# Performance work log

Measured on AMD Instinct MI355X. Metric: run time of the kernel, lower is better.

Reference implementation:

```python
import jax, jax.numpy as jnp
import numpy as np

MIN_V, MAX_V, NORM = 0.0, 4.0, 4.0
NUM_HEADS = 8
BN_EPS = 1e-5

@jax.custom_vjp
def quant(x):
    return jnp.round(jnp.clip(x, MIN_V, MAX_V))

def _quant_fwd(x):
    return jnp.round(jnp.clip(x, MIN_V, MAX_V)), x

def _quant_bwd(x, g):
    # straight-through: zero grad outside [min, max]
    return (jnp.where((x < MIN_V) | (x > MAX_V), 0.0, g),)

quant.defvjp(_quant_fwd, _quant_bwd)

def spike(x):
    return quant(x) / NORM

def conv_bn(x, w, gamma, beta, mean, var):
    # 1x1 conv (no bias) + BatchNorm2d (eval mode, running stats)
    y = jnp.einsum('oc,bchw->bohw', w, x)
    s = gamma / jnp.sqrt(var + BN_EPS)
    return y * s[None, :, None, None] + (beta - mean * s)[None, :, None, None]


def setup_inputs() -> dict:
    key = jax.random.key(0)
    B, C, H, W = 8, 384, 64, 64
    ks = jax.random.split(key, 21)
    d = {'x': jax.random.normal(ks[0], (B, C, H, W), jnp.float32)}
    i = 1
    for p in ('q', 'k', 'v', 'p'):
        d[f'{p}_w'] = jax.random.normal(ks[i], (C, C), jnp.float32) * 0.05; i += 1
        d[f'{p}_gamma'] = jax.random.uniform(ks[i], (C,), jnp.float32, 0.5, 1.5); i += 1
        d[f'{p}_beta'] = jax.random.normal(ks[i], (C,), jnp.float32) * 0.1; i += 1
        d[f'{p}_mean'] = jax.random.normal(ks[i], (C,), jnp.float32) * 0.1; i += 1
        d[f'{p}_var'] = jax.random.uniform(ks[i], (C,), jnp.float32, 0.5, 1.5); i += 1
    return d


def reference(x, q_w, q_gamma, q_beta, q_mean, q_var,
              k_w, k_gamma, k_beta, k_mean, k_var,
              v_w, v_gamma, v_beta, v_mean, v_var,
              p_w, p_gamma, p_beta, p_mean, p_var):
    B, C, H, W = x.shape
    N = H * W
    hd = C // NUM_HEADS
    scale = hd ** -0.5

    xs = spike(x)
    q = spike(conv_bn(xs, q_w, q_gamma, q_beta, q_mean, q_var))
    k = spike(conv_bn(xs, k_w, k_gamma, k_beta, k_mean, k_var))
    v = spike(conv_bn(xs, v_w, v_gamma, v_beta, v_mean, v_var))

    # (B,C,H,W) -> (B,heads,N,hd); channel c = h*hd + d
    def to_heads(t):
        return t.reshape(B, NUM_HEADS, hd, N).transpose(0, 1, 3, 2)

    q, k, v = to_heads(q), to_heads(k), to_heads(v)

    # softmax-free attention: (q @ k^T) @ v == q @ (k^T @ v)  -> O(N*d^2)
    kv = jnp.einsum('bhnd,bhne->bhde', k, v)          # [B,H,hd,hd]
    attn = jnp.einsum('bhnd,bhde->bhne', q, kv) * (scale * 2)  # [B,H,N,hd]

    # back to (B, C_v, N): torch does transpose(2,3).reshape(B,C_v,N)
    a = attn.transpose(0, 1, 3, 2).reshape(B, C, N)
    a = spike(a).reshape(B, C, H, W)
    out = conv_bn(a, p_w, p_gamma, p_beta, p_mean, p_var)
    return out
```

## Files before the change

kernel.cpp:

```cpp
#include <hip/hip_runtime.h>
#include <stdint.h>

#define B_  8
#define C_  384
#define N_  4096
#define NH_ 8
#define HD_ 48
#define CB_ (C_*N_)
#define KS2 768

typedef __attribute__((ext_vector_type(8))) short short8;
typedef __attribute__((ext_vector_type(8))) _Float16 half8;
typedef __attribute__((ext_vector_type(4))) float f32x4;

struct P5 { const float *w, *g, *be, *mu, *va; };
struct W4 { const float *w0, *w1, *w2, *w3; };

__device__ __forceinline__ float b2f(unsigned short u) {
    union { unsigned int i; float f; } c; c.i = ((unsigned int)u) << 16; return c.f;
}
__device__ __forceinline__ unsigned short f2b(float f) {
    union { float f; unsigned int i; } c; c.f = f;
    return (unsigned short)((c.i + 0x7FFFu + ((c.i >> 16) & 1u)) >> 16);
}
__device__ __forceinline__ unsigned short f2h(float f) {
    union { _Float16 h; unsigned short u; } c; c.h = (_Float16)f; return c.u;
}
__device__ __forceinline__ float spikef(float f) {
    f = fminf(fmaxf(f, 0.0f), 4.0f);
    return rintf(f) * 0.25f;
}
__device__ __forceinline__ void async16(const void* g, void* l) {
    __builtin_amdgcn_global_load_lds((const __attribute__((address_space(1))) void*)g,
                                     (__attribute__((address_space(3))) void*)l, 16, 0, 0);
}

__global__ __launch_bounds__(256) void k_prep(W4 ws4, unsigned short* __restrict__ wsp) {
    int idx = blockIdx.x * 256 + threadIdx.x;
    if (idx >= 589824) return;
    int mat = idx / 147456, rem = idx % 147456;
    int o = rem / 384, c = rem % 384;
    const float* W = (mat == 0) ? ws4.w0 : (mat == 1) ? ws4.w1 : (mat == 2) ? ws4.w2 : ws4.w3;
    float w = W[o * 384 + c];
    _Float16 hh = (fabsf(w) < 6.103515625e-05f) ? (_Float16)0 : (_Float16)w;
    float r1 = w - (float)hh;
    float s  = r1 * 4096.0f;
    union { _Float16 h; unsigned short u; } ch, cl;
    ch.h = hh; cl.h = (_Float16)s;
    unsigned short* row = wsp + (size_t)mat * 384 * KS2 + (size_t)o * KS2 + c;
    row[0] = cl.u; row[384] = ch.u;
}

__global__ __launch_bounds__(256) void k0_spike_T(const float* __restrict__ x,
                                                  unsigned short* __restrict__ xst) {
    int nt = blockIdx.x, ct = blockIdx.y, b = blockIdx.z;
    int t = threadIdx.x;
    __shared__ __attribute__((aligned(16))) unsigned short sm[64][68];
    int n0 = nt * 64, c0 = ct * 64;
    const float* xb = x + (size_t)b * CB_;
    #pragma unroll
    for (int i = 0; i < 4; ++i) {
        int c = (t >> 4) + 16 * i;
        int seg = t & 15;
        float4 d = *(const float4*)(xb + (size_t)(c0 + c) * N_ + n0 + seg * 4);
        unsigned short v[4];
        v[0] = f2h(spikef(d.x)); v[1] = f2h(spikef(d.y));
        v[2] = f2h(spikef(d.z)); v[3] = f2h(spikef(d.w));
        *(uint2*)&sm[c][seg * 4] = *(const uint2*)v;
    }
    __syncthreads();
    unsigned short* ob = xst + (size_t)b * CB_;
    #pragma unroll
    for (int i = 0; i < 2; ++i) {
        int flat = i * 256 + t;
        int n = flat >> 3, segc = flat & 7;
        unsigned short v[8];
        #pragma unroll
        for (int j = 0; j < 8; ++j) v[j] = sm[segc * 8 + j][n];
        *(uint4*)(ob + (size_t)(n0 + n) * C_ + c0 + segc * 8) = *(const uint4*)v;
    }
}

__global__ __launch_bounds__(256) void k1_qkv(const unsigned short* __restrict__ xst,
                                              const unsigned short* __restrict__ wsp,
                                              P5 pq, P5 pk, P5 pv,
                                              unsigned short* __restrict__ qs,
                                              unsigned short* __restrict__ ks,
                                              unsigned short* __restrict__ vs) {
    int mt = blockIdx.x, ntile = blockIdx.y, b = blockIdx.z;
    int mat = mt / 3;
    int orow0 = (mt % 3) * 128;
    int n0 = ntile * 128;
    int t = threadIdx.x, lane = t & 63, wvv = t >> 6;
    int wr = wvv >> 1, wc = wvv & 1;

    __shared__ __attribute__((aligned(16))) short lds[17408];
    P5 pp = (mat == 0) ? pq : (mat == 1 ? pk : pv);
    const unsigned short* abase = xst + (size_t)b * CB_;
    const unsigned short* wbase = wsp + (size_t)mat * 384 * KS2;

    f32x4 acc[4][4] = {};
    for (int kk = 0; kk < KS2; kk += 64) {
        if (kk == 384) {
            #pragma unroll
            for (int mi = 0; mi < 4; ++mi)
                #pragma unroll
                for (int ni = 0; ni < 4; ++ni)
                    acc[mi][ni] = acc[mi][ni] * 0.000244140625f;
        }
        int ck = (kk >= 384) ? kk - 384 : kk;
        #pragma unroll
        for (int j = 0; j < 4; ++j) {
            int row = wvv * 32 + j * 8 + (lane >> 3);
            int g = (lane & 7) ^ (row & 7);
            async16(abase + (size_t)(n0 + row) * C_ + ck + g * 8, lds + (wvv * 32 + j * 8) * 64);
        }
        #pragma unroll
        for (int j = 0; j < 4; ++j) {
            int row = wvv * 32 + j * 8 + (lane >> 3);
            int g = (lane & 7) ^ (row & 7);
            async16(wbase + (size_t)(orow0 + row) * KS2 + kk + g * 8, lds + 8192 + (wvv * 32 + j * 8) * 64);
        }
        __syncthreads();
        #pragma unroll
        for (int ksb = 0; ksb < 2; ++ksb) {
            half8 af[4], bfr[4];
            #pragma unroll
            for (int mi = 0; mi < 4; ++mi) {
                int row = wr * 64 + mi * 16 + (lane & 15);
                int s = (ksb * 4 + (lane >> 4)) ^ (row & 7);
                af[mi] = *(const half8*)&lds[row * 64 + s * 8];
            }
            #pragma unroll
            for (int ni = 0; ni < 4; ++ni) {
                int row = wc * 64 + ni * 16 + (lane & 15);
                int s = (ksb * 4 + (lane >> 4)) ^ (row & 7);
                bfr[ni] = *(const half8*)&lds[8192 + row * 64 + s * 8];
            }
            #pragma unroll
            for (int mi = 0; mi < 4; ++mi)
                #pragma unroll
                for (int ni = 0; ni < 4; ++ni)
                    acc[mi][ni] = __builtin_amdgcn_mfma_f32_16x16x32_f16(af[mi], bfr[ni], acc[mi][ni], 0, 0, 0);
        }
        __syncthreads();
    }

    float s_bn[4], t_bn[4];
    #pragma unroll
    for (int ni = 0; ni < 4; ++ni) {
        int o = orow0 + wc * 64 + ni * 16 + (lane & 15);
        float g = pp.g[o], be = pp.be[o], mu = pp.mu[o], va = pp.va[o];
        float s = g / sqrtf(va + 1e-5f);
        s_bn[ni] = s; t_bn[ni] = be - mu * s;
    }
    unsigned short* esm = (unsigned short*)lds;

    if (mat != 0) {
        #pragma unroll
        for (int mi = 0; mi < 4; ++mi)
            #pragma unroll
            for (int ni = 0; ni < 4; ++ni) {
                int ol = wc * 64 + ni * 16 + (lane & 15);
                int nb = wr * 64 + mi * 16 + (lane >> 4) * 4;
                unsigned short vv[4];
                #pragma unroll
                for (int r = 0; r < 4; ++r)
                    vv[r] = f2b(spikef(acc[mi][ni][r] * s_bn[ni] + t_bn[ni]));
                *(uint2*)&esm[ol * 136 + nb] = *(const uint2*)vv;
            }
        __syncthreads();
        unsigned short* dst = ((mat == 1) ? ks : vs) + (size_t)b * CB_;
        #pragma unroll
        for (int i = 0; i < 8; ++i) {
            int o = (t >> 4) + 16 * i;
            int seg = t & 15;
            uint4 d = *(const uint4*)&esm[o * 136 + seg * 8];
            *(uint4*)(dst + (size_t)(orow0 + o) * N_ + n0 + seg * 8) = d;
        }
    } else {
        #pragma unroll
        for (int mi = 0; mi < 4; ++mi)
            #pragma unroll
            for (int ni = 0; ni < 4; ++ni) {
                int ol = wc * 64 + ni * 16 + (lane & 15);
                int nb = wr * 64 + mi * 16 + (lane >> 4) * 4;
                #pragma unroll
                for (int r = 0; r < 4; ++r)
                    esm[(nb + r) * 136 + ol] = f2b(spikef(acc[mi][ni][r] * s_bn[ni] + t_bn[ni]));
            }
        __syncthreads();
        #pragma unroll
        for (int i = 0; i < 8; ++i) {
            int n = (t >> 4) + 16 * i;
            int seg = t & 15;
            uint4 d = *(const uint4*)&esm[n * 136 + seg * 8];
            *(uint4*)(qs + ((size_t)b * N_ + n0 + n) * C_ + orow0 + seg * 8) = d;
        }
    }
}

__global__ __launch_bounds__(256) void k2_kv(const unsigned short* __restrict__ ks,
                                             const unsigned short* __restrict__ vs,
                                             float* __restrict__ kvf) {
    int id = blockIdx.x;
    int b = id >> 5, h = (id >> 2) & 7, ck = id & 3;
    int t = threadIdx.x, lane = t & 63, w = t >> 6;
    const unsigned short* kb = ks + (size_t)b * CB_ + h * HD_ * N_;
    const unsigned short* vb = vs + (size_t)b * CB_ + h * HD_ * N_;
    int kbase = ck * 1024 + w * 256;

    f32x4 acc[3][3] = {};
    for (int kk = 0; kk < 256; kk += 32) {
        int n = kbase + kk + (lane >> 4) * 8;
        short8 af[3], bfr[3];
        #pragma unroll
        for (int di = 0; di < 3; ++di)
            af[di] = *(const short8*)(kb + (size_t)((lane & 15) + 16 * di) * N_ + n);
        #pragma unroll
        for (int ei = 0; ei < 3; ++ei)
            bfr[ei] = *(const short8*)(vb + (size_t)((lane & 15) + 16 * ei) * N_ + n);
        #pragma unroll
        for (int di = 0; di < 3; ++di)
            #pragma unroll
            for (int ei = 0; ei < 3; ++ei)
                acc[di][ei] = __builtin_amdgcn_mfma_f32_16x16x32_bf16(af[di], bfr[ei], acc[di][ei], 0, 0, 0);
    }
    __shared__ float red[4][48][48];
    #pragma unroll
    for (int di = 0; di < 3; ++di)
        #pragma unroll
        for (int ei = 0; ei < 3; ++ei) {
            int d0 = di * 16 + (lane >> 4) * 4;
            int e = ei * 16 + (lane & 15);
            #pragma unroll
            for (int r = 0; r < 4; ++r) red[w][d0 + r][e] = acc[di][ei][r];
        }
    __syncthreads();
    for (int i = t; i < 2304; i += 256) {
        int e = i / 48, d = i % 48;
        float sum = red[0][d][e] + red[1][d][e] + red[2][d][e] + red[3][d][e];
        atomicAdd(&kvf[(b * NH_ + h) * 2304 + e * 48 + d], sum);
    }
}

__global__ __launch_bounds__(256) void k2b_split(const float* __restrict__ kvf,
                                                 unsigned short* __restrict__ hi,
                                                 unsigned short* __restrict__ lo) {
    int i = blockIdx.x * 256 + threadIdx.x;
    if (i >= 64 * 48 * 64) return;
    int d = i & 63; int rest = i >> 6;
    unsigned short h16 = 0, l16 = 0;
    if (d < 48) {
        float v = kvf[rest * 48 + d];
        h16 = f2b(v);
        l16 = f2b(v - b2f(h16));
    }
    hi[i] = h16; lo[i] = l16;
}

__global__ __launch_bounds__(256) void k3_attn(const unsigned short* __restrict__ qs,
                                               const unsigned short* __restrict__ hi,
                                               const unsigned short* __restrict__ lo,
                                               unsigned short* __restrict__ as_) {
    int id = blockIdx.x;
    int b = id >> 6, nt = id & 63;
    int t = threadIdx.x, lane = t & 63, w = t >> 6;
    int n0 = nt * 64 + w * 16;
    const unsigned short* qb = qs + ((size_t)b * N_ + n0) * C_;
    const float S2 = 0.28867513459481287f;

    for (int h = 0; h < NH_; ++h) {
        f32x4 acc[3] = {};
        #pragma unroll
        for (int ksb = 0; ksb < 2; ++ksb) {
            int koff = h * HD_ + ksb * 32 + (lane >> 4) * 8;
            short8 a = *(const short8*)(qb + (size_t)(lane & 15) * C_ + koff);
            #pragma unroll
            for (int ei = 0; ei < 3; ++ei) {
                int e = ei * 16 + (lane & 15);
                size_t boff = ((size_t)(b * NH_ + h) * HD_ + e) * 64 + ksb * 32 + (lane >> 4) * 8;
                short8 bh = *(const short8*)(hi + boff);
                short8 bl = *(const short8*)(lo + boff);
                acc[ei] = __builtin_amdgcn_mfma_f32_16x16x32_bf16(a, bh, acc[ei], 0, 0, 0);
                acc[ei] = __builtin_amdgcn_mfma_f32_16x16x32_bf16(a, bl, acc[ei], 0, 0, 0);
            }
        }
        unsigned short* ab = as_ + ((size_t)b * N_ + n0) * C_ + h * HD_;
        #pragma unroll
        for (int ei = 0; ei < 3; ++ei) {
            int e = ei * 16 + (lane & 15);
            #pragma unroll
            for (int r = 0; r < 4; ++r)
                ab[(size_t)((lane >> 4) * 4 + r) * C_ + e] = f2h(spikef(acc[ei][r] * S2));
        }
    }
}

__global__ __launch_bounds__(256) void k4_pconv(const unsigned short* __restrict__ as_,
                                                const unsigned short* __restrict__ wsp,
                                                P5 pp,
                                                float* __restrict__ out) {
    int mt = blockIdx.x, ntile = blockIdx.y, b = blockIdx.z;
    int orow0 = mt * 128;
    int n0 = ntile * 128;
    int t = threadIdx.x, lane = t & 63, wvv = t >> 6;
    int wr = wvv >> 1, wc = wvv & 1;

    __shared__ __attribute__((aligned(16))) short lds[16384];
    const unsigned short* abase = as_ + (size_t)b * CB_;
    const unsigned short* wbase = wsp + (size_t)3 * 384 * KS2;

    f32x4 acc[4][4] = {};
    for (int kk = 0; kk < KS2; kk += 64) {
        if (kk == 384) {
            #pragma unroll
            for (int mi = 0; mi < 4; ++mi)
                #pragma unroll
                for (int ni = 0; ni < 4; ++ni)
                    acc[mi][ni] = acc[mi][ni] * 0.000244140625f;
        }
        int ck = (kk >= 384) ? kk - 384 : kk;
        #pragma unroll
        for (int j = 0; j < 4; ++j) {
            int row = wvv * 32 + j * 8 + (lane >> 3);
            int g = (lane & 7) ^ (row & 7);
            async16(abase + (size_t)(n0 + row) * C_ + ck + g * 8, lds + (wvv * 32 + j * 8) * 64);
        }
        #pragma unroll
        for (int j = 0; j < 4; ++j) {
            int row = wvv * 32 + j * 8 + (lane >> 3);
            int g = (lane & 7) ^ (row & 7);
            async16(wbase + (size_t)(orow0 + row) * KS2 + kk + g * 8, lds + 8192 + (wvv * 32 + j * 8) * 64);
        }
        __syncthreads();
        #pragma unroll
        for (int ksb = 0; ksb < 2; ++ksb) {
            half8 af[4], bfr[4];
            #pragma unroll
            for (int mi = 0; mi < 4; ++mi) {
                int row = wr * 64 + mi * 16 + (lane & 15);
                int s = (ksb * 4 + (lane >> 4)) ^ (row & 7);
                af[mi] = *(const half8*)&lds[row * 64 + s * 8];
            }
            #pragma unroll
            for (int ni = 0; ni < 4; ++ni) {
                int row = wc * 64 + ni * 16 + (lane & 15);
                int s = (ksb * 4 + (lane >> 4)) ^ (row & 7);
                bfr[ni] = *(const half8*)&lds[8192 + row * 64 + s * 8];
            }
            #pragma unroll
            for (int mi = 0; mi < 4; ++mi)
                #pragma unroll
                for (int ni = 0; ni < 4; ++ni)
                    acc[mi][ni] = __builtin_amdgcn_mfma_f32_16x16x32_f16(af[mi], bfr[ni], acc[mi][ni], 0, 0, 0);
        }
        __syncthreads();
    }

    float s_bn[4], t_bn[4];
    #pragma unroll
    for (int ni = 0; ni < 4; ++ni) {
        int o = orow0 + wc * 64 + ni * 16 + (lane & 15);
        float g = pp.g[o], be = pp.be[o], mu = pp.mu[o], va = pp.va[o];
        float s = g / sqrtf(va + 1e-5f);
        s_bn[ni] = s; t_bn[ni] = be - mu * s;
    }
    #pragma unroll
    for (int mi = 0; mi < 4; ++mi)
        #pragma unroll
        for (int ni = 0; ni < 4; ++ni) {
            int o = orow0 + wc * 64 + ni * 16 + (lane & 15);
            int n = n0 + wr * 64 + mi * 16 + (lane >> 4) * 4;
            f32x4 vv;
            #pragma unroll
            for (int r = 0; r < 4; ++r)
                vv[r] = acc[mi][ni][r] * s_bn[ni] + t_bn[ni];
            *(f32x4*)(out + ((size_t)b * C_ + o) * N_ + n) = vv;
        }
}

extern "C" void kernel_launch(void* const* d_in, const int* in_sizes, int n_in,
                              void* d_out, int out_size, void* d_ws, size_t ws_size,
                              hipStream_t stream) {
    P5 pq { (const float*)d_in[1],  (const float*)d_in[2],  (const float*)d_in[3],
            (const float*)d_in[4],  (const float*)d_in[5] };
    P5 pk { (const float*)d_in[6],  (const float*)d_in[7],  (const float*)d_in[8],
            (const float*)d_in[9],  (const float*)d_in[10] };
    P5 pv { (const float*)d_in[11], (const float*)d_in[12], (const float*)d_in[13],
            (const float*)d_in[14], (const float*)d_in[15] };
    P5 pp { (const float*)d_in[16], (const float*)d_in[17], (const float*)d_in[18],
            (const float*)d_in[19], (const float*)d_in[20] };
    W4 w4 { pq.w, pk.w, pv.w, pp.w };

    char* ws = (char*)d_ws;
    const size_t S = (size_t)B_ * C_ * N_ * 2;
    unsigned short* xst = (unsigned short*)ws;
    unsigned short* qs  = (unsigned short*)(ws + S);
    unsigned short* ks  = (unsigned short*)(ws + 2 * S + 256);
    unsigned short* vs  = (unsigned short*)(ws + 3 * S + 512);
    float*          kvf = (float*)(ws + 4 * S + 768);
    unsigned short* hi  = (unsigned short*)(ws + 4 * S + 768 + 589824);
    unsigned short* lo  = (unsigned short*)(ws + 4 * S + 768 + 589824 + 393216);
    unsigned short* wsp = (unsigned short*)(ws + 4 * S + 768 + 589824 + 2 * 393216);
    unsigned short* as_ = xst;

    hipMemsetAsync(kvf, 0, 589824, stream);
    k_prep<<<2304, 256, 0, stream>>>(w4, wsp);
    k0_spike_T<<<dim3(64, 6, 8), 256, 0, stream>>>((const float*)d_in[0], xst);
    k1_qkv<<<dim3(9, 32, 8), 256, 0, stream>>>(xst, wsp, pq, pk, pv, qs, ks, vs);
    k2_kv<<<256, 256, 0, stream>>>(ks, vs, kvf);
    k2b_split<<<768, 256, 0, stream>>>(kvf, hi, lo);
    k3_attn<<<512, 256, 0, stream>>>(qs, hi, lo, as_);
    k4_pconv<<<dim3(3, 32, 8), 256, 0, stream>>>(as_, wsp, pp, (float*)d_out);
}
```

Before: 294.9 us.

## Fuse hi/lo weight passes, XCD-aware block mapping, finer kv split, staged attn stores

The QKV and projection GEMMs now load the A tile once per K step and run the hi and lo weight MFMAs against it with two accumulators, instead of streaming A twice over a doubled K loop. Blocks are remapped so that tiles sharing the same activation rows land on the same XCD, which should improve L2 reuse. The kv reduction kernel is split into four times as many blocks to raise parallelism, at the cost of more atomic traffic. The attention kernel stages its output in LDS and writes coalesced 16-byte rows. Holding two accumulator sets raises register use and LDS grows, which may lower occupancy.

```diff
diff --git a/kernel.cpp b/kernel.cpp
--- a/kernel.cpp
+++ b/kernel.cpp
@@ -87,33 +87,29 @@
                                               unsigned short* __restrict__ qs,
                                               unsigned short* __restrict__ ks,
                                               unsigned short* __restrict__ vs) {
-    int mt = blockIdx.x, ntile = blockIdx.y, b = blockIdx.z;
+    int gid = blockIdx.x;
+    int xcd = gid & 7, idx = gid >> 3;
+    int pairSlot = idx / 9, mt = idx - pairSlot * 9;
+    int p = xcd * 32 + pairSlot;
+    int ntile = p >> 3, b = p & 7;
     int mat = mt / 3;
     int orow0 = (mt % 3) * 128;
     int n0 = ntile * 128;
     int t = threadIdx.x, lane = t & 63, wvv = t >> 6;
     int wr = wvv >> 1, wc = wvv & 1;
 
-    __shared__ __attribute__((aligned(16))) short lds[17408];
+    __shared__ __attribute__((aligned(16))) short lds[24576];
     P5 pp = (mat == 0) ? pq : (mat == 1 ? pk : pv);
     const unsigned short* abase = xst + (size_t)b * CB_;
     const unsigned short* wbase = wsp + (size_t)mat * 384 * KS2;
 
-    f32x4 acc[4][4] = {};
-    for (int kk = 0; kk < KS2; kk += 64) {
-        if (kk == 384) {
-            #pragma unroll
-            for (int mi = 0; mi < 4; ++mi)
-                #pragma unroll
-                for (int ni = 0; ni < 4; ++ni)
-                    acc[mi][ni] = acc[mi][ni] * 0.000244140625f;
-        }
-        int ck = (kk >= 384) ? kk - 384 : kk;
-        #pragma unroll
-        for (int j = 0; j < 4; ++j) {
-            int row = wvv * 32 + j * 8 + (lane >> 3);
-            int g = (lane & 7) ^ (row & 7);
-            async16(abase + (size_t)(n0 + row) * C_ + ck + g * 8, lds + (wvv * 32 + j * 8) * 64);
+    f32x4 accH[4][4] = {}, accL[4][4] = {};
+    for (int kk = 0; kk < 384; kk += 64) {
+        #pragma unroll
+        for (int j = 0; j < 4; ++j) {
+            int row = wvv * 32 + j * 8 + (lane >> 3);
+            int g = (lane & 7) ^ (row & 7);
+            async16(abase + (size_t)(n0 + row) * C_ + kk + g * 8, lds + (wvv * 32 + j * 8) * 64);
         }
         #pragma unroll
         for (int j = 0; j < 4; ++j) {
@@ -121,10 +117,16 @@
             int g = (lane & 7) ^ (row & 7);
             async16(wbase + (size_t)(orow0 + row) * KS2 + kk + g * 8, lds + 8192 + (wvv * 32 + j * 8) * 64);
         }
+        #pragma unroll
+        for (int j = 0; j < 4; ++j) {
+            int row = wvv * 32 + j * 8 + (lane >> 3);
+            int g = (lane & 7) ^ (row & 7);
+            async16(wbase + (size_t)(orow0 + row) * KS2 + 384 + kk + g * 8, lds + 16384 + (wvv * 32 + j * 8) * 64);
+        }
         __syncthreads();
         #pragma unroll
         for (int ksb = 0; ksb < 2; ++ksb) {
-            half8 af[4], bfr[4];
+            half8 af[4], bl[4], bh[4];
             #pragma unroll
             for (int mi = 0; mi < 4; ++mi) {
                 int row = wr * 64 + mi * 16 + (lane & 15);
@@ -135,13 +137,16 @@
             for (int ni = 0; ni < 4; ++ni) {
                 int row = wc * 64 + ni * 16 + (lane & 15);
                 int s = (ksb * 4 + (lane >> 4)) ^ (row & 7);
-                bfr[ni] = *(const half8*)&lds[8192 + row * 64 + s * 8];
+                bl[ni] = *(const half8*)&lds[8192 + row * 64 + s * 8];
+                bh[ni] = *(const half8*)&lds[16384 + row * 64 + s * 8];
             }
             #pragma unroll
             for (int mi = 0; mi < 4; ++mi)
                 #pragma unroll
-                for (int ni = 0; ni < 4; ++ni)
-                    acc[mi][ni] = __builtin_amdgcn_mfma_f32_16x16x32_f16(af[mi], bfr[ni], acc[mi][ni], 0, 0, 0);
+                for (int ni = 0; ni < 4; ++ni) {
+                    accL[mi][ni] = __builtin_amdgcn_mfma_f32_16x16x32_f16(af[mi], bl[ni], accL[mi][ni], 0, 0, 0);
+                    accH[mi][ni] = __builtin_amdgcn_mfma_f32_16x16x32_f16(af[mi], bh[ni], accH[mi][ni], 0, 0, 0);
+                }
         }
         __syncthreads();
     }
@@ -165,8 +170,10 @@
                 int nb = wr * 64 + mi * 16 + (lane >> 4) * 4;
                 unsigned short vv[4];
                 #pragma unroll
-                for (int r = 0; r < 4; ++r)
-                    vv[r] = f2b(spikef(acc[mi][ni][r] * s_bn[ni] + t_bn[ni]));
+                for (int r = 0; r < 4; ++r) {
+                    float v = accH[mi][ni][r] + accL[mi][ni][r] * 0.000244140625f;
+                    vv[r] = f2b(spikef(v * s_bn[ni] + t_bn[ni]));
+                }
                 *(uint2*)&esm[ol * 136 + nb] = *(const uint2*)vv;
             }
         __syncthreads();
@@ -186,8 +193,10 @@
                 int ol = wc * 64 + ni * 16 + (lane & 15);
                 int nb = wr * 64 + mi * 16 + (lane >> 4) * 4;
                 #pragma unroll
-                for (int r = 0; r < 4; ++r)
-                    esm[(nb + r) * 136 + ol] = f2b(spikef(acc[mi][ni][r] * s_bn[ni] + t_bn[ni]));
+                for (int r = 0; r < 4; ++r) {
+                    float v = accH[mi][ni][r] + accL[mi][ni][r] * 0.000244140625f;
+                    esm[(nb + r) * 136 + ol] = f2b(spikef(v * s_bn[ni] + t_bn[ni]));
+                }
             }
         __syncthreads();
         #pragma unroll
@@ -204,14 +213,15 @@
                                              const unsigned short* __restrict__ vs,
                                              float* __restrict__ kvf) {
     int id = blockIdx.x;
-    int b = id >> 5, h = (id >> 2) & 7, ck = id & 3;
+    int b = id >> 7, h = (id >> 4) & 7, ck = id & 15;
     int t = threadIdx.x, lane = t & 63, w = t >> 6;
     const unsigned short* kb = ks + (size_t)b * CB_ + h * HD_ * N_;
     const unsigned short* vb = vs + (size_t)b * CB_ + h * HD_ * N_;
-    int kbase = ck * 1024 + w * 256;
+    int kbase = ck * 256 + w * 64;
 
     f32x4 acc[3][3] = {};
-    for (int kk = 0; kk < 256; kk += 32) {
+    #pragma unroll
+    for (int kk = 0; kk < 64; kk += 32) {
         int n = kbase + kk + (lane >> 4) * 8;
         short8 af[3], bfr[3];
         #pragma unroll
@@ -266,9 +276,11 @@
     int id = blockIdx.x;
     int b = id >> 6, nt = id & 63;
     int t = threadIdx.x, lane = t & 63, w = t >> 6;
-    int n0 = nt * 64 + w * 16;
+    int nb0 = nt * 64;
+    int n0 = nb0 + w * 16;
     const unsigned short* qb = qs + ((size_t)b * N_ + n0) * C_;
     const float S2 = 0.28867513459481287f;
+    __shared__ __attribute__((aligned(16))) unsigned short sm[64][392];
 
     for (int h = 0; h < NH_; ++h) {
         f32x4 acc[3] = {};
@@ -286,14 +298,22 @@
                 acc[ei] = __builtin_amdgcn_mfma_f32_16x16x32_bf16(a, bl, acc[ei], 0, 0, 0);
             }
         }
-        unsigned short* ab = as_ + ((size_t)b * N_ + n0) * C_ + h * HD_;
         #pragma unroll
         for (int ei = 0; ei < 3; ++ei) {
             int e = ei * 16 + (lane & 15);
             #pragma unroll
             for (int r = 0; r < 4; ++r)
-                ab[(size_t)((lane >> 4) * 4 + r) * C_ + e] = f2h(spikef(acc[ei][r] * S2));
-        }
+                sm[w * 16 + (lane >> 4) * 4 + r][h * HD_ + e] = f2h(spikef(acc[ei][r] * S2));
+        }
+    }
+    __syncthreads();
+    unsigned short* ob = as_ + ((size_t)b * N_ + nb0) * C_;
+    #pragma unroll
+    for (int i = 0; i < 12; ++i) {
+        int f = i * 256 + t;
+        int row = f / 48, seg = f % 48;
+        uint4 d = *(const uint4*)&sm[row][seg * 8];
+        *(uint4*)(ob + (size_t)row * C_ + seg * 8) = d;
     }
 }
 
@@ -301,31 +321,27 @@
                                                 const unsigned short* __restrict__ wsp,
                                                 P5 pp,
                                                 float* __restrict__ out) {
-    int mt = blockIdx.x, ntile = blockIdx.y, b = blockIdx.z;
+    int gid = blockIdx.x;
+    int xcd = gid & 7, idx = gid >> 3;
+    int pairSlot = idx / 3, mt = idx - pairSlot * 3;
+    int p = xcd * 32 + pairSlot;
+    int ntile = p >> 3, b = p & 7;
     int orow0 = mt * 128;
     int n0 = ntile * 128;
     int t = threadIdx.x, lane = t & 63, wvv = t >> 6;
     int wr = wvv >> 1, wc = wvv & 1;
 
-    __shared__ __attribute__((aligned(16))) short lds[16384];
+    __shared__ __attribute__((aligned(16))) short lds[24576];
     const unsigned short* abase = as_ + (size_t)b * CB_;
     const unsigned short* wbase = wsp + (size_t)3 * 384 * KS2;
 
-    f32x4 acc[4][4] = {};
-    for (int kk = 0; kk < KS2; kk += 64) {
-        if (kk == 384) {
-            #pragma unroll
-            for (int mi = 0; mi < 4; ++mi)
-                #pragma unroll
-                for (int ni = 0; ni < 4; ++ni)
-                    acc[mi][ni] = acc[mi][ni] * 0.000244140625f;
-        }
-        int ck = (kk >= 384) ? kk - 384 : kk;
-        #pragma unroll
-        for (int j = 0; j < 4; ++j) {
-            int row = wvv * 32 + j * 8 + (lane >> 3);
-            int g = (lane & 7) ^ (row & 7);
-            async16(abase + (size_t)(n0 + row) * C_ + ck + g * 8, lds + (wvv * 32 + j * 8) * 64);
+    f32x4 accH[4][4] = {}, accL[4][4] = {};
+    for (int kk = 0; kk < 384; kk += 64) {
+        #pragma unroll
+        for (int j = 0; j < 4; ++j) {
+            int row = wvv * 32 + j * 8 + (lane >> 3);
+            int g = (lane & 7) ^ (row & 7);
+            async16(abase + (size_t)(n0 + row) * C_ + kk + g * 8, lds + (wvv * 32 + j * 8) * 64);
         }
         #pragma unroll
         for (int j = 0; j < 4; ++j) {
@@ -333,10 +349,16 @@
             int g = (lane & 7) ^ (row & 7);
             async16(wbase + (size_t)(orow0 + row) * KS2 + kk + g * 8, lds + 8192 + (wvv * 32 + j * 8) * 64);
         }
+        #pragma unroll
+        for (int j = 0; j < 4; ++j) {
+            int row = wvv * 32 + j * 8 + (lane >> 3);
+            int g = (lane & 7) ^ (row & 7);
+            async16(wbase + (size_t)(orow0 + row) * KS2 + 384 + kk + g * 8, lds + 16384 + (wvv * 32 + j * 8) * 64);
+        }
         __syncthreads();
         #pragma unroll
         for (int ksb = 0; ksb < 2; ++ksb) {
-            half8 af[4], bfr[4];
+            half8 af[4], bl[4], bh[4];
             #pragma unroll
             for (int mi = 0; mi < 4; ++mi) {
                 int row = wr * 64 + mi * 16 + (lane & 15);
@@ -347,13 +369,16 @@
             for (int ni = 0; ni < 4; ++ni) {
                 int row = wc * 64 + ni * 16 + (lane & 15);
                 int s = (ksb * 4 + (lane >> 4)) ^ (row & 7);
-                bfr[ni] = *(const half8*)&lds[8192 + row * 64 + s * 8];
+                bl[ni] = *(const half8*)&lds[8192 + row * 64 + s * 8];
+                bh[ni] = *(const half8*)&lds[16384 + row * 64 + s * 8];
             }
             #pragma unroll
             for (int mi = 0; mi < 4; ++mi)
                 #pragma unroll
-                for (int ni = 0; ni < 4; ++ni)
-                    acc[mi][ni] = __builtin_amdgcn_mfma_f32_16x16x32_f16(af[mi], bfr[ni], acc[mi][ni], 0, 0, 0);
+                for (int ni = 0; ni < 4; ++ni) {
+                    accL[mi][ni] = __builtin_amdgcn_mfma_f32_16x16x32_f16(af[mi], bl[ni], accL[mi][ni], 0, 0, 0);
+                    accH[mi][ni] = __builtin_amdgcn_mfma_f32_16x16x32_f16(af[mi], bh[ni], accH[mi][ni], 0, 0, 0);
+                }
         }
         __syncthreads();
     }
@@ -374,8 +399,10 @@
             int n = n0 + wr * 64 + mi * 16 + (lane >> 4) * 4;
             f32x4 vv;
             #pragma unroll
-            for (int r = 0; r < 4; ++r)
-                vv[r] = acc[mi][ni][r] * s_bn[ni] + t_bn[ni];
+            for (int r = 0; r < 4; ++r) {
+                float v = accH[mi][ni][r] + accL[mi][ni][r] * 0.000244140625f;
+                vv[r] = v * s_bn[ni] + t_bn[ni];
+            }
             *(f32x4*)(out + ((size_t)b * C_ + o) * N_ + n) = vv;
         }
 }
@@ -408,9 +435,9 @@
     hipMemsetAsync(kvf, 0, 589824, stream);
     k_prep<<<2304, 256, 0, stream>>>(w4, wsp);
     k0_spike_T<<<dim3(64, 6, 8), 256, 0, stream>>>((const float*)d_in[0], xst);
-    k1_qkv<<<dim3(9, 32, 8), 256, 0, stream>>>(xst, wsp, pq, pk, pv, qs, ks, vs);
-    k2_kv<<<256, 256, 0, stream>>>(ks, vs, kvf);
+    k1_qkv<<<2304, 256, 0, stream>>>(xst, wsp, pq, pk, pv, qs, ks, vs);
+    k2_kv<<<1024, 256, 0, stream>>>(ks, vs, kvf);
     k2b_split<<<768, 256, 0, stream>>>(kvf, hi, lo);
     k3_attn<<<512, 256, 0, stream>>>(qs, hi, lo, as_);
-    k4_pconv<<<dim3(3, 32, 8), 256, 0, stream>>>(as_, wsp, pp, (float*)d_out);
-}
+    k4_pconv<<<768, 256, 0, stream>>>(as_, wsp, pp, (float*)d_out);
+}
```

Measured after the change: 330.2 us. 1.12x slower.

## Remap GEMM blocks per XCD, split kv reduction finer, stage attn output in LDS

Applied to the files above, without the earlier changes.

k1 and k4 switch to a 1D grid whose block index is decoded so that all M-tiles sharing one (ntile,b) activation tile land on the same XCD, aiming for better L2 reuse. k2 splits the N reduction into 16 chunks instead of 4 (1024 blocks), raising parallelism at the cost of more atomic accumulation traffic. k3 writes the spiked attention output into a shared-memory tile and then stores full 16-byte rows coalesced, replacing the scattered 2-byte global stores, at the cost of extra LDS and a barrier.

```diff
diff --git a/kernel.cpp b/kernel.cpp
--- a/kernel.cpp
+++ b/kernel.cpp
@@ -87,7 +87,11 @@
                                               unsigned short* __restrict__ qs,
                                               unsigned short* __restrict__ ks,
                                               unsigned short* __restrict__ vs) {
-    int mt = blockIdx.x, ntile = blockIdx.y, b = blockIdx.z;
+    int gid = blockIdx.x;
+    int xcd = gid & 7, idx = gid >> 3;
+    int pairSlot = idx / 9, mt = idx - pairSlot * 9;
+    int p = xcd * 32 + pairSlot;
+    int ntile = p >> 3, b = p & 7;
     int mat = mt / 3;
     int orow0 = (mt % 3) * 128;
     int n0 = ntile * 128;
@@ -204,14 +208,15 @@
                                              const unsigned short* __restrict__ vs,
                                              float* __restrict__ kvf) {
     int id = blockIdx.x;
-    int b = id >> 5, h = (id >> 2) & 7, ck = id & 3;
+    int b = id >> 7, h = (id >> 4) & 7, ck = id & 15;
     int t = threadIdx.x, lane = t & 63, w = t >> 6;
     const unsigned short* kb = ks + (size_t)b * CB_ + h * HD_ * N_;
     const unsigned short* vb = vs + (size_t)b * CB_ + h * HD_ * N_;
-    int kbase = ck * 1024 + w * 256;
+    int kbase = ck * 256 + w * 64;
 
     f32x4 acc[3][3] = {};
-    for (int kk = 0; kk < 256; kk += 32) {
+    #pragma unroll
+    for (int kk = 0; kk < 64; kk += 32) {
         int n = kbase + kk + (lane >> 4) * 8;
         short8 af[3], bfr[3];
         #pragma unroll
@@ -266,9 +271,11 @@
     int id = blockIdx.x;
     int b = id >> 6, nt = id & 63;
     int t = threadIdx.x, lane = t & 63, w = t >> 6;
-    int n0 = nt * 64 + w * 16;
+    int nb0 = nt * 64;
+    int n0 = nb0 + w * 16;
     const unsigned short* qb = qs + ((size_t)b * N_ + n0) * C_;
     const float S2 = 0.28867513459481287f;
+    __shared__ __attribute__((aligned(16))) unsigned short sm[64][392];
 
     for (int h = 0; h < NH_; ++h) {
         f32x4 acc[3] = {};
@@ -286,14 +293,22 @@
                 acc[ei] = __builtin_amdgcn_mfma_f32_16x16x32_bf16(a, bl, acc[ei], 0, 0, 0);
             }
         }
-        unsigned short* ab = as_ + ((size_t)b * N_ + n0) * C_ + h * HD_;
         #pragma unroll
         for (int ei = 0; ei < 3; ++ei) {
             int e = ei * 16 + (lane & 15);
             #pragma unroll
             for (int r = 0; r < 4; ++r)
-                ab[(size_t)((lane >> 4) * 4 + r) * C_ + e] = f2h(spikef(acc[ei][r] * S2));
-        }
+                sm[w * 16 + (lane >> 4) * 4 + r][h * HD_ + e] = f2h(spikef(acc[ei][r] * S2));
+        }
+    }
+    __syncthreads();
+    unsigned short* ob = as_ + ((size_t)b * N_ + nb0) * C_;
+    #pragma unroll
+    for (int i = 0; i < 12; ++i) {
+        int f = i * 256 + t;
+        int row = f / 48, seg = f % 48;
+        uint4 d = *(const uint4*)&sm[row][seg * 8];
+        *(uint4*)(ob + (size_t)row * C_ + seg * 8) = d;
     }
 }
 
@@ -301,7 +316,11 @@
                                                 const unsigned short* __restrict__ wsp,
                                                 P5 pp,
                                                 float* __restrict__ out) {
-    int mt = blockIdx.x, ntile = blockIdx.y, b = blockIdx.z;
+    int gid = blockIdx.x;
+    int xcd = gid & 7, idx = gid >> 3;
+    int pairSlot = idx / 3, mt = idx - pairSlot * 3;
+    int p = xcd * 32 + pairSlot;
+    int ntile = p >> 3, b = p & 7;
     int orow0 = mt * 128;
     int n0 = ntile * 128;
     int t = threadIdx.x, lane = t & 63, wvv = t >> 6;
@@ -408,9 +427,9 @@
     hipMemsetAsync(kvf, 0, 589824, stream);
     k_prep<<<2304, 256, 0, stream>>>(w4, wsp);
     k0_spike_T<<<dim3(64, 6, 8), 256, 0, stream>>>((const float*)d_in[0], xst);
-    k1_qkv<<<dim3(9, 32, 8), 256, 0, stream>>>(xst, wsp, pq, pk, pv, qs, ks, vs);
-    k2_kv<<<256, 256, 0, stream>>>(ks, vs, kvf);
+    k1_qkv<<<2304, 256, 0, stream>>>(xst, wsp, pq, pk, pv, qs, ks, vs);
+    k2_kv<<<1024, 256, 0, stream>>>(ks, vs, kvf);
     k2b_split<<<768, 256, 0, stream>>>(kvf, hi, lo);
     k3_attn<<<512, 256, 0, stream>>>(qs, hi, lo, as_);
-    k4_pconv<<<dim3(3, 32, 8), 256, 0, stream>>>(as_, wsp, pp, (float*)d_out);
-}
+    k4_pconv<<<768, 256, 0, stream>>>(as_, wsp, pp, (float*)d_out);
+}
```

Result: faster. 272.0 us (-7.8%).
